# Kernel tuning notes

Hardware: AMD Instinct MI355X
Metric: run time of the kernel (lower is better)

## Reference

```python
import jax, jax.numpy as jnp
import numpy as np

B, T, N_EMBD = 4, 2048, 1024
NUM_EXPERTS, TOP_K = 8, 2
N_CITIES = 4
LIN = N_EMBD + 32 + N_EMBD // 4 + N_EMBD // 4 + N_EMBD // 8 + N_EMBD // 8  # 1824


def setup_inputs() -> dict:
    key = jax.random.key(0)
    ks = jax.random.split(key, 12)
    s = 0.02  # init std as in _init_weights
    return {
        "x": jax.random.normal(ks[0], (B, T, N_EMBD), jnp.float32),
        "delta_t_info": jax.random.normal(ks[1], (B, T, N_EMBD // 4), jnp.float32),
        "delta_dis_info": jax.random.normal(ks[2], (B, T, N_EMBD // 4), jnp.float32),
        "delta_rg_info": jax.random.normal(ks[3], (B, T, N_EMBD // 8), jnp.float32),
        "delta_entropy_info": jax.random.normal(ks[4], (B, T, N_EMBD // 8), jnp.float32),
        "city_embeddings": jax.random.normal(ks[5], (N_CITIES, 32), jnp.float32),
        "Wg": jax.random.normal(ks[6], (LIN, NUM_EXPERTS), jnp.float32) * s,
        "bg": jnp.zeros((NUM_EXPERTS,), jnp.float32),
        "W1": jax.random.normal(ks[7], (NUM_EXPERTS, N_EMBD, 4 * N_EMBD), jnp.float32) * s,
        "b1": jnp.zeros((NUM_EXPERTS, 4 * N_EMBD), jnp.float32),
        "W2": jax.random.normal(ks[8], (NUM_EXPERTS, 4 * N_EMBD, N_EMBD), jnp.float32) * s,
        "b2": jnp.zeros((NUM_EXPERTS, N_EMBD), jnp.float32),
        "city_index": 1,
    }


def _moe(x, dt, dd, drg, de, city_embeddings, Wg, bg, W1, b1, W2, b2, city_index):
    b, t, _ = x.shape
    city = jnp.broadcast_to(city_embeddings[city_index], (b, t, 32))
    feats = jnp.concatenate([x, city, dt, dd, drg, de], axis=-1)  # [B,T,LIN]
    logits = jnp.einsum("btl,le->bte", feats, Wg) + bg            # eval mode: no noise
    gate1 = jax.nn.softmax(logits, axis=-1)
    _, topi = jax.lax.top_k(logits, TOP_K)                        # [B,T,k]
    # mask of top-k experts per token; scatter(-inf elsewhere) + softmax
    mask = jax.nn.one_hot(topi, NUM_EXPERTS, dtype=jnp.float32).sum(axis=-2) > 0
    sparse_logits = jnp.where(mask, logits, -jnp.inf)
    gates = jax.nn.softmax(sparse_logits, axis=-1)                # zeros outside top-k
    out = jnp.zeros_like(x)
    for e in range(NUM_EXPERTS):  # fixed small expert set
        h = jax.nn.gelu(jnp.einsum("btc,ch->bth", x, W1[e]) + b1[e], approximate=True)
        y = jnp.einsum("bth,hc->btc", h, W2[e]) + b2[e]
        out = out + gates[..., e:e + 1] * y  # gate is exactly 0 for non-topk tokens
    return out, gate1


def reference(x, delta_t_info, delta_dis_info, delta_rg_info, delta_entropy_info,
              city_embeddings, Wg, bg, W1, b1, W2, b2, city_index):
    return _moe(x, delta_t_info, delta_dis_info, delta_rg_info, delta_entropy_info,
                city_embeddings, Wg, bg, W1, b1, W2, b2, city_index)
```

## Files before the change

### kernel.cpp

```cpp
#include <hip/hip_runtime.h>
#include <hip/hip_bf16.h>
#include <stdint.h>

#define NTOK 8192
#define DEMB 1024
#define HDIM 4096
#define NEXP 8
#define LINF 1824
#define MAXPAD 18432

typedef __attribute__((ext_vector_type(8))) __bf16 bf16x8;
typedef __attribute__((ext_vector_type(4))) __bf16 bf16x4v;
typedef __attribute__((ext_vector_type(4))) float f32x4;

__device__ __forceinline__ void gload_lds16(const void* g, void* l) {
  __builtin_amdgcn_global_load_lds(
      (const __attribute__((address_space(1))) void*)g,
      (__attribute__((address_space(3))) void*)l, 16, 0, 0);
}

__device__ __forceinline__ float dot4(float4 a, float4 b) {
  return a.x*b.x + a.y*b.y + a.z*b.z + a.w*b.w;
}

__global__ void __launch_bounds__(256) k_logits(
    const float* __restrict__ x, const float* __restrict__ dt,
    const float* __restrict__ dd, const float* __restrict__ drg,
    const float* __restrict__ de, const float* __restrict__ city,
    const float* __restrict__ Wg, const float* __restrict__ bg,
    const int* __restrict__ city_index,
    float* __restrict__ gate1, int* __restrict__ top_i, float2* __restrict__ top_g,
    __bf16* __restrict__ xb)
{
  __shared__ float WgT[NEXP * LINF];
  const int tid = threadIdx.x;
  const float4* Wg4 = (const float4*)Wg;
  for (int i = tid; i < LINF * NEXP / 4; i += 256) {
    float4 v = Wg4[i];
    int e0 = (i & 1) * 4, f = i >> 1;
    WgT[(e0+0)*LINF + f] = v.x; WgT[(e0+1)*LINF + f] = v.y;
    WgT[(e0+2)*LINF + f] = v.z; WgT[(e0+3)*LINF + f] = v.w;
  }
  __syncthreads();

  const int wave = tid >> 6, lane = tid & 63;
  const int ci = city_index[0];
  const float4* city4 = (const float4*)(city + ci*32);
  const float4 z4 = {0.f, 0.f, 0.f, 0.f};

  #pragma unroll
  for (int k = 0; k < 4; ++k) {
    const int t = blockIdx.x*16 + wave*4 + k;
    const float4* x4 = (const float4*)x + (size_t)t*256;
    float4 xv0 = x4[lane], xv1 = x4[64+lane], xv2 = x4[128+lane], xv3 = x4[192+lane];

    {
      bf16x4v* xrow = (bf16x4v*)(xb + (size_t)t*1024);
      bf16x4v o0, o1, o2, o3;
      o0[0]=(__bf16)xv0.x; o0[1]=(__bf16)xv0.y; o0[2]=(__bf16)xv0.z; o0[3]=(__bf16)xv0.w;
      o1[0]=(__bf16)xv1.x; o1[1]=(__bf16)xv1.y; o1[2]=(__bf16)xv1.z; o1[3]=(__bf16)xv1.w;
      o2[0]=(__bf16)xv2.x; o2[1]=(__bf16)xv2.y; o2[2]=(__bf16)xv2.z; o2[3]=(__bf16)xv2.w;
      o3[0]=(__bf16)xv3.x; o3[1]=(__bf16)xv3.y; o3[2]=(__bf16)xv3.z; o3[3]=(__bf16)xv3.w;
      xrow[lane] = o0; xrow[64+lane] = o1; xrow[128+lane] = o2; xrow[192+lane] = o3;
    }

    float4 cv = (lane < 8) ? city4[lane] : z4;
    float4 tv = ((const float4*)dt)[(size_t)t*64 + lane];
    float4 dv = ((const float4*)dd)[(size_t)t*64 + lane];
    float4 rv = z4, ev = z4;
    if (lane < 32) {
      rv = ((const float4*)drg)[(size_t)t*32 + lane];
      ev = ((const float4*)de )[(size_t)t*32 + lane];
    }
    float a[8];
    const int l8 = lane & 7, l32 = lane & 31;
    #pragma unroll
    for (int e = 0; e < 8; ++e) {
      const float4* W = (const float4*)(WgT + e*LINF);
      float s = dot4(xv0, W[lane]) + dot4(xv1, W[64+lane])
              + dot4(xv2, W[128+lane]) + dot4(xv3, W[192+lane]);
      s += dot4(cv, W[256 + l8]);
      s += dot4(tv, W[264 + lane]) + dot4(dv, W[328 + lane]);
      s += dot4(rv, W[392 + l32]) + dot4(ev, W[424 + l32]);
      a[e] = s;
    }
    #pragma unroll
    for (int off = 32; off > 0; off >>= 1)
      #pragma unroll
      for (int e = 0; e < 8; ++e) a[e] += __shfl_xor(a[e], off);

    float lg[8];
    #pragma unroll
    for (int e = 0; e < 8; ++e) lg[e] = a[e] + bg[e];
    float mx = lg[0];
    #pragma unroll
    for (int e = 1; e < 8; ++e) mx = fmaxf(mx, lg[e]);
    float ex[8]; float s = 0.f;
    #pragma unroll
    for (int e = 0; e < 8; ++e) { ex[e] = expf(lg[e] - mx); s += ex[e]; }
    int i1 = 0; float l1 = lg[0];
    #pragma unroll
    for (int e = 1; e < 8; ++e) if (lg[e] > l1) { l1 = lg[e]; i1 = e; }
    int i2 = -1; float l2 = -1e30f;
    #pragma unroll
    for (int e = 0; e < 8; ++e) if (e != i1 && lg[e] > l2) { l2 = lg[e]; i2 = e; }
    float e2 = expf(l2 - l1);

    if (lane == 0) {
      float inv = 1.f / s;
      float4 o0 = { ex[0]*inv, ex[1]*inv, ex[2]*inv, ex[3]*inv };
      float4 o1 = { ex[4]*inv, ex[5]*inv, ex[6]*inv, ex[7]*inv };
      float4* gp = (float4*)(gate1 + (size_t)t*8);
      gp[0] = o0; gp[1] = o1;
      top_i[t] = i1 | (i2 << 4);
      float2 g = { 1.f / (1.f + e2), e2 / (1.f + e2) };
      top_g[t] = g;
    }
  }
}

__global__ void __launch_bounds__(256) k_build(
    const int* __restrict__ top_i, const float2* __restrict__ top_g,
    int* __restrict__ counts, int* __restrict__ ex_tok, float* __restrict__ ex_gate,
    int2* __restrict__ ppos)
{
  __shared__ int lcnt[8], lbase[8];
  const int tid = threadIdx.x;
  if (tid < 8) lcnt[tid] = 0;
  __syncthreads();
  const int t = blockIdx.x*256 + tid;
  const int ti = top_i[t];
  const int i1 = ti & 15, i2 = ti >> 4;
  const float2 g = top_g[t];
  int p1 = atomicAdd(&lcnt[i1], 1);
  int p2 = atomicAdd(&lcnt[i2], 1);
  __syncthreads();
  if (tid < 8) lbase[tid] = atomicAdd(&counts[tid], lcnt[tid]);
  __syncthreads();
  int s1 = lbase[i1] + p1; ex_tok[i1*NTOK+s1] = t; ex_gate[i1*NTOK+s1] = g.x;
  int s2 = lbase[i2] + p2; ex_tok[i2*NTOK+s2] = t; ex_gate[i2*NTOK+s2] = g.y;
  int2 pp = { i1 | (s1 << 3), i2 | (s2 << 3) };
  ppos[t] = pp;
}

__global__ void k_finalize(const int* __restrict__ counts, int* __restrict__ seg) {
  if (threadIdx.x == 0 && blockIdx.x == 0) {
    int s = 0;
    for (int e = 0; e < 8; ++e) { seg[e] = s; s += (counts[e] + 255) & ~255; }
    seg[8] = s;
  }
}

template<int RDIM, int CDIM>
__global__ void __launch_bounds__(256) k_tconv(
    const float* __restrict__ W, __bf16* __restrict__ WT)
{
  const int e  = blockIdx.z;
  const int c0 = blockIdx.x * 64, r0 = blockIdx.y * 64;
  __shared__ float tb[64 * 65];
  const float* src = W  + (size_t)e * RDIM * CDIM + (size_t)r0 * CDIM + c0;
  __bf16*      dst = WT + (size_t)e * RDIM * CDIM + (size_t)c0 * RDIM + r0;
  const int tx = threadIdx.x & 15, ty = threadIdx.x >> 4;
  #pragma unroll
  for (int i = 0; i < 4; ++i) {
    int r = ty + i*16;
    float4 v = *(const float4*)(src + (size_t)r*CDIM + tx*4);
    tb[(tx*4+0)*65 + r] = v.x; tb[(tx*4+1)*65 + r] = v.y;
    tb[(tx*4+2)*65 + r] = v.z; tb[(tx*4+3)*65 + r] = v.w;
  }
  __syncthreads();
  const int sg = threadIdx.x & 7, dr8 = threadIdx.x >> 3;
  #pragma unroll
  for (int i = 0; i < 2; ++i) {
    int d = dr8 + i*32;
    const float* row = tb + d*65 + sg*8;
    bf16x8 o;
    #pragma unroll
    for (int j = 0; j < 8; ++j) o[j] = (__bf16)row[j];
    *(bf16x8*)(dst + (size_t)d*RDIM + sg*8) = o;
  }
}

template<int KDIM, int KFULL, int NDIM, bool G1>
__global__ void __launch_bounds__(256, 2) k_moe_gemm(
    const __bf16* __restrict__ Abase, const __bf16* __restrict__ WT,
    const float* __restrict__ bias,
    const int* __restrict__ seg, const int* __restrict__ counts,
    const int* __restrict__ ex_tok,
    int chunk0, __bf16* __restrict__ dstbuf)
{
  constexpr int NT = KDIM / 64;
  const int nx = gridDim.x, ny = gridDim.y, nz = gridDim.z;
  const int total = nx * ny * nz;
  int flat;
  if (G1) flat = blockIdx.x + nx * blockIdx.y;
  else    flat = blockIdx.y + ny * (blockIdx.x + nx * blockIdx.z);
  { int q = total >> 3, r = total & 7; int xcd = flat & 7, idx = flat >> 3;
    flat = (xcd < r ? xcd*(q+1) : r*(q+1) + (xcd-r)*q) + idx; }
  int bx, by, bz;
  if (G1) { bx = flat % nx; by = flat / nx; bz = 0; }
  else    { by = flat % ny; int f2 = flat / ny; bx = f2 % nx; bz = f2 / nx; }

  const int segtot = seg[8];
  const int row0 = chunk0 + bx * 128;
  if (row0 >= segtot) return;
  int e = 0;
  #pragma unroll
  for (int qq = 1; qq < 8; ++qq) if (row0 >= seg[qq]) e = qq;
  const int cnt = counts[e], sege = seg[e];
  const int n0 = by * 128;
  const int kbase = bz * KDIM;

  __shared__ __align__(16) char smem[65536];

  const int tid = threadIdx.x;
  const int wid = tid >> 6, lane = tid & 63;
  const int wm = wid >> 1, wn = wid & 1;
  const int l15 = lane & 15, l4 = lane >> 4;
  const __bf16* Bsrc = WT + (size_t)e * NDIM * KFULL;

  float bv[4];
  if (G1) {
    #pragma unroll
    for (int N = 0; N < 4; ++N)
      bv[N] = bias[(size_t)e*NDIM + n0 + wn*64 + N*16 + l15];
    asm volatile("" :: "v"(bv[0]), "v"(bv[1]), "v"(bv[2]), "v"(bv[3]));
  }

  const __bf16* sp[4][2];
  #pragma unroll
  for (int j = 0; j < 2; ++j) {
    int g = j*256 + tid;
    int sl = g >> 3;
    int kb = (g & 7) ^ (sl & 7);
    #pragma unroll
    for (int mh = 0; mh < 2; ++mh) {
      int R = mh*64 + sl;
      int arow;
      if (G1) { int lr = row0 + R - sege; arow = (lr < cnt) ? ex_tok[e*NTOK + lr] : 0; }
      else    { arow = row0 + R - chunk0; }
      sp[mh][j] = Abase + (size_t)arow * KFULL + kbase + kb*8;
    }
    #pragma unroll
    for (int nh = 0; nh < 2; ++nh) {
      int C = nh*64 + sl;
      sp[2+nh][j] = Bsrc + (size_t)(n0 + C) * KFULL + kbase + kb*8;
    }
  }

  int xo[2];
  #pragma unroll
  for (int kk = 0; kk < 2; ++kk) xo[kk] = (((kk*4 + l4) ^ (l15 & 7)) * 16);
  int arb[4], brb[4];
  #pragma unroll
  for (int m = 0; m < 4; ++m) arb[m] = wm*8192 + (m*16 + l15) * 128;
  #pragma unroll
  for (int n = 0; n < 4; ++n) brb[n] = 16384 + wn*8192 + (n*16 + l15) * 128;

  auto ISSUE = [&](int h, int tt) {
    char* b = smem + (tt & 1) * 32768 + h * 8192;
    gload_lds16(sp[h][0] + tt*64, b + tid*16);
    gload_lds16(sp[h][1] + tt*64, b + 256*16 + tid*16);
  };

  f32x4 acc[4][4] = {};

  ISSUE(0,0); ISSUE(1,0); ISSUE(2,0); ISSUE(3,0);
  asm volatile("s_waitcnt vmcnt(0)" ::: "memory");
  __builtin_amdgcn_s_barrier();

  for (int t = 0; t < NT; ++t) {
    const char* cb = smem + (t & 1) * 32768;
    if (t + 1 < NT) {
      ISSUE(0, t+1); ISSUE(1, t+1); ISSUE(2, t+1); ISSUE(3, t+1);
    }
    bf16x8 af[4][2], bfv[4][2];
    #pragma unroll
    for (int m = 0; m < 4; ++m)
      #pragma unroll
      for (int kk = 0; kk < 2; ++kk)
        af[m][kk] = *(const bf16x8*)(cb + arb[m] + xo[kk]);
    #pragma unroll
    for (int n = 0; n < 4; ++n)
      #pragma unroll
      for (int kk = 0; kk < 2; ++kk)
        bfv[n][kk] = *(const bf16x8*)(cb + brb[n] + xo[kk]);
    __builtin_amdgcn_s_setprio(1);
    #pragma unroll
    for (int m = 0; m < 4; ++m)
      #pragma unroll
      for (int n = 0; n < 4; ++n)
        #pragma unroll
        for (int kk = 0; kk < 2; ++kk)
          acc[m][n] = __builtin_amdgcn_mfma_f32_16x16x32_bf16(af[m][kk], bfv[n][kk], acc[m][n], 0, 0, 0);
    __builtin_amdgcn_s_setprio(0);
    asm volatile("s_waitcnt vmcnt(0)" ::: "memory");
    __builtin_amdgcn_s_barrier();
  }

  __bf16* Cl = (__bf16*)smem;
  #pragma unroll
  for (int M = 0; M < 4; ++M) {
    #pragma unroll
    for (int N = 0; N < 4; ++N) {
      #pragma unroll
      for (int r2 = 0; r2 < 4; ++r2) {
        float v = acc[M][N][r2];
        if (G1) {
          v += bv[N];
          float z = 2.302208f * (v + 0.044715f * v * v * v);
          v = v / (1.f + exp2f(-z));
        }
        Cl[(wm*64 + M*16 + l4*4 + r2)*128 + wn*64 + N*16 + l15] = (__bf16)v;
      }
    }
  }
  __syncthreads();
  const int drow0 = G1 ? (row0 - chunk0) : row0;
  __bf16* dst = dstbuf + (G1 ? (size_t)0 : (size_t)bz * MAXPAD * NDIM);
  #pragma unroll
  for (int it = 0; it < 8; ++it) {
    int idx2 = it*256 + tid;
    int rr = idx2 >> 4, c8 = (idx2 & 15) * 8;
    *(bf16x8*)(dst + (size_t)(drow0 + rr)*NDIM + n0 + c8) =
        *(const bf16x8*)(Cl + rr*128 + c8);
  }
}

__global__ void __launch_bounds__(256) k_combine(
    const __bf16* __restrict__ pbuf, const int2* __restrict__ ppos,
    const float2* __restrict__ top_g, const int* __restrict__ seg,
    const float* __restrict__ b2, float* __restrict__ out)
{
  const int t = blockIdx.x, tid = threadIdx.x;
  const int2 pp = ppos[t];
  const float2 g = top_g[t];
  const int e1 = pp.x & 7, i1 = pp.x >> 3;
  const int e2 = pp.y & 7, i2 = pp.y >> 3;
  const size_t r1 = (size_t)(seg[e1] + i1) * DEMB;
  const size_t r2 = (size_t)(seg[e2] + i2) * DEMB;
  const int c = tid * 4;
  float4 ba = *(const float4*)(b2 + (size_t)e1*DEMB + c);
  float4 bb = *(const float4*)(b2 + (size_t)e2*DEMB + c);
  float s1x = ba.x, s1y = ba.y, s1z = ba.z, s1w = ba.w;
  float s2x = bb.x, s2y = bb.y, s2z = bb.z, s2w = bb.w;
  #pragma unroll
  for (int p = 0; p < 2; ++p) {
    const __bf16* pb = pbuf + (size_t)p * MAXPAD * DEMB;
    bf16x4v a = *(const bf16x4v*)(pb + r1 + c);
    bf16x4v b = *(const bf16x4v*)(pb + r2 + c);
    s1x += (float)a[0]; s1y += (float)a[1]; s1z += (float)a[2]; s1w += (float)a[3];
    s2x += (float)b[0]; s2y += (float)b[1]; s2z += (float)b[2]; s2w += (float)b[3];
  }
  float4 o;
  o.x = g.x*s1x + g.y*s2x;
  o.y = g.x*s1y + g.y*s2y;
  o.z = g.x*s1z + g.y*s2z;
  o.w = g.x*s1w + g.y*s2w;
  *(float4*)(out + (size_t)t*DEMB + c) = o;
}

extern "C" void kernel_launch(void* const* d_in, const int* in_sizes, int n_in,
                              void* d_out, int out_size, void* d_ws, size_t ws_size,
                              hipStream_t stream)
{
  const float* x   = (const float*)d_in[0];
  const float* dt  = (const float*)d_in[1];
  const float* dd  = (const float*)d_in[2];
  const float* drg = (const float*)d_in[3];
  const float* de  = (const float*)d_in[4];
  const float* city= (const float*)d_in[5];
  const float* Wg  = (const float*)d_in[6];
  const float* bg  = (const float*)d_in[7];
  const float* W1  = (const float*)d_in[8];
  const float* b1  = (const float*)d_in[9];
  const float* W2  = (const float*)d_in[10];
  const float* b2  = (const float*)d_in[11];
  const int* city_index = (const int*)d_in[12];

  float* out   = (float*)d_out;
  float* gate1 = out + (size_t)NTOK * DEMB;

  char* p = (char*)d_ws;
  int*    counts  = (int*)p;      p += 256;
  int*    seg     = (int*)p;      p += 256;
  int*    top_i   = (int*)p;      p += (size_t)NTOK*4;
  float2* top_g   = (float2*)p;   p += (size_t)NTOK*8;
  int2*   ppos    = (int2*)p;     p += (size_t)NTOK*8;
  int*    ex_tok  = (int*)p;      p += (size_t)NTOK*NEXP*4;
  float*  ex_gate = (float*)p;    p += (size_t)NTOK*NEXP*4;
  __bf16* xb      = (__bf16*)p;   p += (size_t)NTOK*DEMB*2;
  __bf16* W1T     = (__bf16*)p;   p += (size_t)NEXP*DEMB*HDIM*2;
  __bf16* W2T     = (__bf16*)p;   p += (size_t)NEXP*DEMB*HDIM*2;
  __bf16* pbuf    = (__bf16*)p;   p += (size_t)2*MAXPAD*DEMB*2;
  __bf16* hbuf    = (__bf16*)p;

  size_t fixed = (size_t)(p - (char*)d_ws);
  int CH = MAXPAD;
  while (CH > 0 && fixed + (size_t)CH * HDIM * 2 > ws_size) CH -= 256;
  if (CH <= 0) return;
  int nch = (MAXPAD + CH - 1) / CH;

  (void)hipMemsetAsync(counts, 0, 64, stream);

  k_tconv<DEMB, HDIM><<<dim3(HDIM/64, DEMB/64, NEXP), 256, 0, stream>>>(W1, W1T);
  k_tconv<HDIM, DEMB><<<dim3(DEMB/64, HDIM/64, NEXP), 256, 0, stream>>>(W2, W2T);

  k_logits<<<NTOK/16, 256, 0, stream>>>(x, dt, dd, drg, de, city, Wg, bg,
                                        city_index, gate1, top_i, top_g, xb);
  k_build<<<NTOK/256, 256, 0, stream>>>(top_i, top_g, counts, ex_tok, ex_gate, ppos);
  k_finalize<<<1, 64, 0, stream>>>(counts, seg);

  for (int c = 0; c < nch; ++c) {
    k_moe_gemm<1024, 1024, HDIM, true><<<dim3(CH/128, HDIM/128, 1), 256, 0, stream>>>(
        xb, W1T, b1, seg, counts, ex_tok, c*CH, hbuf);
    k_moe_gemm<2048, 4096, DEMB, false><<<dim3(CH/128, DEMB/128, 2), 256, 0, stream>>>(
        hbuf, W2T, b2, seg, counts, ex_tok, c*CH, pbuf);
  }
  k_combine<<<NTOK, 256, 0, stream>>>(pbuf, ppos, top_g, seg, b2, out);
}
```

Measured before the change: 562.0 us.

## Halve GEMM K-tile to 32 to cut LDS and raise occupancy to 4 blocks

The MoE GEMM K-step drops from 64 to 32, halving shared memory to 32KB, and launch bounds now allow 4 blocks per CU instead of 2. The LDS swizzle and addressing are rewritten for 64-byte rows. The aim is more resident waves to hide load latency. In exchange there are twice as many loop iterations and barriers per tile, fewer MFMAs between syncs, and a tighter register budget that could cause spills with the 64-float accumulator.

Result: slower. 576.5 us (+2.6%).

```diff
diff --git a/kernel.cpp b/kernel.cpp
--- a/kernel.cpp
+++ b/kernel.cpp
@@ -182,14 +182,14 @@
 }
 
 template<int KDIM, int KFULL, int NDIM, bool G1>
-__global__ void __launch_bounds__(256, 2) k_moe_gemm(
+__global__ void __launch_bounds__(256, 4) k_moe_gemm(
     const __bf16* __restrict__ Abase, const __bf16* __restrict__ WT,
     const float* __restrict__ bias,
     const int* __restrict__ seg, const int* __restrict__ counts,
     const int* __restrict__ ex_tok,
     int chunk0, __bf16* __restrict__ dstbuf)
 {
-  constexpr int NT = KDIM / 64;
+  constexpr int NT = KDIM / 32;
   const int nx = gridDim.x, ny = gridDim.y, nz = gridDim.z;
   const int total = nx * ny * nz;
   int flat;
@@ -211,7 +211,7 @@
   const int n0 = by * 128;
   const int kbase = bz * KDIM;
 
-  __shared__ __align__(16) char smem[65536];
+  __shared__ __align__(16) char smem[32768];
 
   const int tid = threadIdx.x;
   const int wid = tid >> 6, lane = tid & 63;
@@ -227,72 +227,55 @@
     asm volatile("" :: "v"(bv[0]), "v"(bv[1]), "v"(bv[2]), "v"(bv[3]));
   }
 
-  const __bf16* sp[4][2];
+  const __bf16* spA[2]; const __bf16* spB[2];
   #pragma unroll
   for (int j = 0; j < 2; ++j) {
     int g = j*256 + tid;
-    int sl = g >> 3;
-    int kb = (g & 7) ^ (sl & 7);
-    #pragma unroll
-    for (int mh = 0; mh < 2; ++mh) {
-      int R = mh*64 + sl;
-      int arow;
-      if (G1) { int lr = row0 + R - sege; arow = (lr < cnt) ? ex_tok[e*NTOK + lr] : 0; }
-      else    { arow = row0 + R - chunk0; }
-      sp[mh][j] = Abase + (size_t)arow * KFULL + kbase + kb*8;
-    }
-    #pragma unroll
-    for (int nh = 0; nh < 2; ++nh) {
-      int C = nh*64 + sl;
-      sp[2+nh][j] = Bsrc + (size_t)(n0 + C) * KFULL + kbase + kb*8;
-    }
-  }
-
-  int xo[2];
-  #pragma unroll
-  for (int kk = 0; kk < 2; ++kk) xo[kk] = (((kk*4 + l4) ^ (l15 & 7)) * 16);
+    int sl = g >> 2;
+    int kb = (g & 3) ^ ((g >> 3) & 3);
+    int arow;
+    if (G1) { int lr = row0 + sl - sege; arow = (lr < cnt) ? ex_tok[e*NTOK + lr] : 0; }
+    else    { arow = row0 + sl - chunk0; }
+    spA[j] = Abase + (size_t)arow * KFULL + kbase + kb*8;
+    spB[j] = Bsrc  + (size_t)(n0 + sl) * KFULL + kbase + kb*8;
+  }
+
+  const int xo = (l4 ^ ((l15 >> 1) & 3)) * 16;
   int arb[4], brb[4];
   #pragma unroll
-  for (int m = 0; m < 4; ++m) arb[m] = wm*8192 + (m*16 + l15) * 128;
-  #pragma unroll
-  for (int n = 0; n < 4; ++n) brb[n] = 16384 + wn*8192 + (n*16 + l15) * 128;
-
-  auto ISSUE = [&](int h, int tt) {
-    char* b = smem + (tt & 1) * 32768 + h * 8192;
-    gload_lds16(sp[h][0] + tt*64, b + tid*16);
-    gload_lds16(sp[h][1] + tt*64, b + 256*16 + tid*16);
+  for (int m = 0; m < 4; ++m) arb[m] = (wm*64 + m*16 + l15) * 64 + xo;
+  #pragma unroll
+  for (int n = 0; n < 4; ++n) brb[n] = 8192 + (wn*64 + n*16 + l15) * 64 + xo;
+
+  auto ISSUE = [&](int tt) {
+    char* b = smem + (tt & 1) * 16384;
+    #pragma unroll
+    for (int j = 0; j < 2; ++j) {
+      gload_lds16(spA[j] + tt*32, b + (j*256 + tid)*16);
+      gload_lds16(spB[j] + tt*32, b + 8192 + (j*256 + tid)*16);
+    }
   };
 
   f32x4 acc[4][4] = {};
 
-  ISSUE(0,0); ISSUE(1,0); ISSUE(2,0); ISSUE(3,0);
+  ISSUE(0);
   asm volatile("s_waitcnt vmcnt(0)" ::: "memory");
   __builtin_amdgcn_s_barrier();
 
   for (int t = 0; t < NT; ++t) {
-    const char* cb = smem + (t & 1) * 32768;
-    if (t + 1 < NT) {
-      ISSUE(0, t+1); ISSUE(1, t+1); ISSUE(2, t+1); ISSUE(3, t+1);
-    }
-    bf16x8 af[4][2], bfv[4][2];
-    #pragma unroll
-    for (int m = 0; m < 4; ++m)
-      #pragma unroll
-      for (int kk = 0; kk < 2; ++kk)
-        af[m][kk] = *(const bf16x8*)(cb + arb[m] + xo[kk]);
-    #pragma unroll
-    for (int n = 0; n < 4; ++n)
-      #pragma unroll
-      for (int kk = 0; kk < 2; ++kk)
-        bfv[n][kk] = *(const bf16x8*)(cb + brb[n] + xo[kk]);
+    const char* cb = smem + (t & 1) * 16384;
+    if (t + 1 < NT) ISSUE(t + 1);
+    bf16x8 af[4], bfv[4];
+    #pragma unroll
+    for (int m = 0; m < 4; ++m) af[m]  = *(const bf16x8*)(cb + arb[m]);
+    #pragma unroll
+    for (int n = 0; n < 4; ++n) bfv[n] = *(const bf16x8*)(cb + brb[n]);
     __builtin_amdgcn_s_setprio(1);
     #pragma unroll
     for (int m = 0; m < 4; ++m)
       #pragma unroll
       for (int n = 0; n < 4; ++n)
-        #pragma unroll
-        for (int kk = 0; kk < 2; ++kk)
-          acc[m][n] = __builtin_amdgcn_mfma_f32_16x16x32_bf16(af[m][kk], bfv[n][kk], acc[m][n], 0, 0, 0);
+        acc[m][n] = __builtin_amdgcn_mfma_f32_16x16x32_bf16(af[m], bfv[n], acc[m][n], 0, 0, 0);
     __builtin_amdgcn_s_setprio(0);
     asm volatile("s_waitcnt vmcnt(0)" ::: "memory");
     __builtin_amdgcn_s_barrier();
```
